# Kernel optimization log

Hardware: AMD Instinct MI355X
Metric: run time of the kernel (lower is better)

Reference implementation:

```python
import jax, jax.numpy as jnp
import numpy as np

D = 768
B = 512

def setup_inputs() -> dict:
    key = jax.random.key(0)
    k1, k2, k3 = jax.random.split(key, 3)
    v_x = jax.random.normal(k1, (B, D), dtype=jnp.float32)
    s_x = jax.random.normal(k2, (B, D), dtype=jnp.float32)
    # nn.Linear(D*D, 2) weight (2, D*D), bias (2,)
    fc_w = jax.random.normal(k3, (2, D * D), dtype=jnp.float32) * 0.01
    fc_b = jnp.zeros((2,), dtype=jnp.float32)
    return {"v_x": v_x, "s_x": s_x, "fc_w": fc_w, "fc_b": fc_b}

def reference(v_x, s_x, fc_w, fc_b):
    d = v_x.shape[1]
    # Original: M[b,i,j] = v_x[b,i]*s_x[b,j]; logits = M_flat @ fc_w.T + fc_b.
    # Equivalent bilinear form avoiding the (B,d,d) intermediate:
    # logits[b,k] = sum_ij v[b,i] * s[b,j] * fc_w[k, i*d+j]
    W = fc_w.reshape(2, d, d)  # W[k,i,j]
    logits = jnp.einsum('bi,kij,bj->bk', v_x, W, s_x) + fc_b
    weights = jax.nn.softmax(logits, axis=-1)
    a = weights[:, 0:1]
    b = weights[:, 1:2]
    fused_x = a * v_x + b * s_x
    return fused_x
```

## Files before the change

### kernel.cpp

```cpp
#include <hip/hip_runtime.h>

#define D 768
#define B 512

#define BM 128
#define BN 128
#define IC 16
#define ISPLIT 16
#define ILEN (D / ISPLIT)
#define NJT (D / BN)
#define NPART (ISPLIT * NJT)
#define WROW 192
#define VROW 132

__global__ __launch_bounds__(256, 4)
void gemm_kernel(const float* __restrict__ v_x,
                 const float* __restrict__ s_x,
                 const float* __restrict__ fc_w,
                 float* __restrict__ partial )
{
    __shared__ float wS[IC * WROW];
    __shared__ float vT[IC * VROW];

    const int tid   = threadIdx.x;
    const int gx    = blockIdx.x;
    const int gy    = blockIdx.y;
    const int gz    = blockIdx.z;
    const int k     = gx / NJT;
    const int jmod  = gx % NJT;
    const int jbase = jmod * BN;
    const int b0    = gy * BM;

    const int jt = tid & 15;
    const int bt = tid >> 4;

    const float* __restrict__ Wk = fc_w + (size_t)k * D * D;

    float acc[8][8];
#pragma unroll
    for (int m = 0; m < 8; ++m)
#pragma unroll
        for (int n = 0; n < 8; ++n) acc[m][n] = 0.f;

    for (int ch = 0; ch < ILEN / IC; ++ch) {
        const int i0 = gz * ILEN + ch * IC;

#pragma unroll
        for (int p = 0; p < 2; ++p) {
            int q  = tid + 256 * p;
            int r  = q >> 5;
            int c4 = q & 31;
            float4 t = *reinterpret_cast<const float4*>(
                &Wk[(size_t)(i0 + r) * D + jbase + c4 * 4]);
            *reinterpret_cast<float4*>(&wS[r * WROW + (c4 >> 1) * 12 + (c4 & 1) * 4]) = t;
        }
#pragma unroll
        for (int p = 0; p < 2; ++p) {
            int q  = tid + 256 * p;
            int bq = q >> 2;
            int c4 = q & 3;
            float4 t = *reinterpret_cast<const float4*>(
                &v_x[(size_t)(b0 + bq) * D + i0 + c4 * 4]);
            vT[(c4 * 4 + 0) * VROW + bq] = t.x;
            vT[(c4 * 4 + 1) * VROW + bq] = t.y;
            vT[(c4 * 4 + 2) * VROW + bq] = t.z;
            vT[(c4 * 4 + 3) * VROW + bq] = t.w;
        }
        __syncthreads();

#pragma unroll
        for (int ii = 0; ii < IC; ++ii) {
            float4 a0 = *reinterpret_cast<const float4*>(&vT[ii * VROW + bt * 8]);
            float4 a1 = *reinterpret_cast<const float4*>(&vT[ii * VROW + bt * 8 + 4]);
            float4 w0 = *reinterpret_cast<const float4*>(&wS[ii * WROW + jt * 12]);
            float4 w1 = *reinterpret_cast<const float4*>(&wS[ii * WROW + jt * 12 + 4]);
            float a8[8] = {a0.x, a0.y, a0.z, a0.w, a1.x, a1.y, a1.z, a1.w};
            float w8[8] = {w0.x, w0.y, w0.z, w0.w, w1.x, w1.y, w1.z, w1.w};
#pragma unroll
            for (int m = 0; m < 8; ++m)
#pragma unroll
                for (int n = 0; n < 8; ++n)
                    acc[m][n] = fmaf(a8[m], w8[n], acc[m][n]);
        }
        __syncthreads();
    }

#pragma unroll
    for (int m = 0; m < 8; ++m) {
        const int row = b0 + bt * 8 + m;
        const float* sp = s_x + (size_t)row * D + jbase + jt * 8;
        float4 s0 = *reinterpret_cast<const float4*>(sp);
        float4 s1 = *reinterpret_cast<const float4*>(sp + 4);
        float val = acc[m][0]*s0.x + acc[m][1]*s0.y + acc[m][2]*s0.z + acc[m][3]*s0.w
                  + acc[m][4]*s1.x + acc[m][5]*s1.y + acc[m][6]*s1.z + acc[m][7]*s1.w;
        val += __shfl_xor(val, 1);
        val += __shfl_xor(val, 2);
        val += __shfl_xor(val, 4);
        val += __shfl_xor(val, 8);
        if (jt == 0) {
            partial[(size_t)row * (2 * NPART) + k * NPART + gz * NJT + jmod] = val;
        }
    }
}

__global__ __launch_bounds__(192)
void fuse_kernel(const float* __restrict__ v_x,
                 const float* __restrict__ s_x,
                 const float* __restrict__ partial,
                 const float* __restrict__ fc_b,
                 float* __restrict__ out)
{
    __shared__ float slog[2];
    const int b    = blockIdx.x;
    const int t    = threadIdx.x;
    const int wave = t >> 6;
    const int lane = t & 63;

    if (wave < 2) {
        const float* P = partial + (size_t)b * (2 * NPART) + wave * NPART;
        float val = P[lane];
        if (lane < NPART - 64) val += P[64 + lane];
        val += __shfl_xor(val, 1);
        val += __shfl_xor(val, 2);
        val += __shfl_xor(val, 4);
        val += __shfl_xor(val, 8);
        val += __shfl_xor(val, 16);
        val += __shfl_xor(val, 32);
        if (lane == 0) slog[wave] = val + fc_b[wave];
    }
    __syncthreads();

    const float l0 = slog[0], l1 = slog[1];
    const float mx = fmaxf(l0, l1);
    const float e0 = __expf(l0 - mx);
    const float e1 = __expf(l1 - mx);
    const float inv = 1.f / (e0 + e1);
    const float wa = e0 * inv;
    const float wb = e1 * inv;

    const float4* v4 = reinterpret_cast<const float4*>(v_x + (size_t)b * D);
    const float4* s4 = reinterpret_cast<const float4*>(s_x + (size_t)b * D);
    float4* o4 = reinterpret_cast<float4*>((float*)out + (size_t)b * D);
    float4 vv = v4[t], ss = s4[t], oo;
    oo.x = wa * vv.x + wb * ss.x;
    oo.y = wa * vv.y + wb * ss.y;
    oo.z = wa * vv.z + wb * ss.z;
    oo.w = wa * vv.w + wb * ss.w;
    o4[t] = oo;
}

extern "C" void kernel_launch(void* const* d_in, const int* in_sizes, int n_in,
                              void* d_out, int out_size, void* d_ws, size_t ws_size,
                              hipStream_t stream) {
    const float* v_x  = (const float*)d_in[0];
    const float* s_x  = (const float*)d_in[1];
    const float* fc_w = (const float*)d_in[2];
    const float* fc_b = (const float*)d_in[3];
    float* out     = (float*)d_out;
    float* partial = (float*)d_ws;

    dim3 g1(2 * NJT, B / BM, ISPLIT);
    gemm_kernel<<<g1, 256, 0, stream>>>(v_x, s_x, fc_w, partial);

    fuse_kernel<<<B, 192, 0, stream>>>(v_x, s_x, partial, fc_b, out);
}
```

Baseline: 85.78 us.

## Use fp16 MFMA for bilinear GEMM with transposed half-precision weights

Adds a prep kernel that converts v_x to fp16 and transposes the two weight matrices into fp16 with a shared-memory tile. The main GEMM then runs on MFMA 16x16x32 f16 instructions with a 64x128 tile and an 8-way K split, reduces across waves through LDS, and writes 48 partials per class instead of 96. This removes the scalar FP32 FMA bottleneck and halves operand bandwidth. In exchange it adds an extra kernel launch plus weight conversion on every call, and rounding inputs to fp16 lowers accuracy.

Measured after the change: 79.99 us. 6.8% less time.

```diff
diff --git a/kernel.cpp b/kernel.cpp
--- a/kernel.cpp
+++ b/kernel.cpp
@@ -3,103 +3,142 @@
 #define D 768
 #define B 512
 
-#define BM 128
+typedef _Float16 half8 __attribute__((ext_vector_type(8)));
+typedef float floatx4 __attribute__((ext_vector_type(4)));
+
+__global__ __launch_bounds__(256)
+void prep_kernel(const float* __restrict__ v_x,
+                 const float* __restrict__ fc_w,
+                 _Float16* __restrict__ WT,
+                 _Float16* __restrict__ v16)
+{
+    __shared__ _Float16 tile[32 * 33];
+    const int bid = blockIdx.x;
+    const int t   = threadIdx.x;
+
+    if (bid < 1152) {
+        const int cls = bid / 576;
+        const int r2  = bid % 576;
+        const int kt  = r2 / 24;
+        const int jt  = r2 % 24;
+        const float* Wc = fc_w + (size_t)cls * D * D;
+        const int r  = t >> 3;
+        const int c4 = t & 7;
+        float4 f = *reinterpret_cast<const float4*>(
+            &Wc[(size_t)(kt * 32 + r) * D + jt * 32 + c4 * 4]);
+        tile[r * 33 + c4 * 4 + 0] = (_Float16)f.x;
+        tile[r * 33 + c4 * 4 + 1] = (_Float16)f.y;
+        tile[r * 33 + c4 * 4 + 2] = (_Float16)f.z;
+        tile[r * 33 + c4 * 4 + 3] = (_Float16)f.w;
+        __syncthreads();
+        alignas(8) _Float16 o[4];
+#pragma unroll
+        for (int e = 0; e < 4; ++e) o[e] = tile[(c4 * 4 + e) * 33 + r];
+        *reinterpret_cast<short4*>(
+            &WT[((size_t)cls * D + jt * 32 + r) * D + kt * 32 + c4 * 4]) =
+            *reinterpret_cast<short4*>(o);
+    } else {
+        const int b2 = bid - 1152;
+        const int base = b2 * 1024 + t * 4;
+        float4 f = *reinterpret_cast<const float4*>(&v_x[base]);
+        alignas(8) _Float16 o[4] = {(_Float16)f.x, (_Float16)f.y,
+                                    (_Float16)f.z, (_Float16)f.w};
+        *reinterpret_cast<short4*>(&v16[base]) = *reinterpret_cast<short4*>(o);
+    }
+}
+
+#define BM 64
 #define BN 128
-#define IC 16
-#define ISPLIT 16
-#define ILEN (D / ISPLIT)
-#define NJT (D / BN)
-#define NPART (ISPLIT * NJT)
-#define WROW 192
-#define VROW 132
-
-__global__ __launch_bounds__(256, 4)
-void gemm_kernel(const float* __restrict__ v_x,
+#define KC 96
+#define LROW 104
+#define NJT 6
+#define NPART 48
+
+__global__ __launch_bounds__(256, 3)
+void gemm_kernel(const _Float16* __restrict__ v16,
+                 const _Float16* __restrict__ WT,
                  const float* __restrict__ s_x,
-                 const float* __restrict__ fc_w,
                  float* __restrict__ partial )
 {
-    __shared__ float wS[IC * WROW];
-    __shared__ float vT[IC * VROW];
-
-    const int tid   = threadIdx.x;
-    const int gx    = blockIdx.x;
-    const int gy    = blockIdx.y;
-    const int gz    = blockIdx.z;
-    const int k     = gx / NJT;
-    const int jmod  = gx % NJT;
-    const int jbase = jmod * BN;
-    const int b0    = gy * BM;
-
-    const int jt = tid & 15;
-    const int bt = tid >> 4;
-
-    const float* __restrict__ Wk = fc_w + (size_t)k * D * D;
-
-    float acc[8][8];
-#pragma unroll
-    for (int m = 0; m < 8; ++m)
-#pragma unroll
-        for (int n = 0; n < 8; ++n) acc[m][n] = 0.f;
-
-    for (int ch = 0; ch < ILEN / IC; ++ch) {
-        const int i0 = gz * ILEN + ch * IC;
-
-#pragma unroll
-        for (int p = 0; p < 2; ++p) {
-            int q  = tid + 256 * p;
-            int r  = q >> 5;
-            int c4 = q & 31;
-            float4 t = *reinterpret_cast<const float4*>(
-                &Wk[(size_t)(i0 + r) * D + jbase + c4 * 4]);
-            *reinterpret_cast<float4*>(&wS[r * WROW + (c4 >> 1) * 12 + (c4 & 1) * 4]) = t;
+    __shared__ _Float16 Alds[BM * LROW];
+    __shared__ _Float16 Blds[BN * LROW];
+    __shared__ float    red[BM * 4];
+
+    const int tid = threadIdx.x;
+    const int jb  = blockIdx.x;
+    const int b0  = blockIdx.y * BM;
+    const int gz  = blockIdx.z;
+    const int kc0 = gz * KC;
+
+    const int w    = tid >> 6;
+    const int lane = tid & 63;
+    const int li   = lane & 15;
+    const int g    = lane >> 4;
+
+#pragma unroll
+    for (int p = 0; p < 3; ++p) {
+        int q   = tid + 256 * p;
+        int row = q / 12, ksl = q % 12;
+        half8 h = *reinterpret_cast<const half8*>(
+            &v16[(size_t)(b0 + row) * D + kc0 + ksl * 8]);
+        *reinterpret_cast<half8*>(&Alds[row * LROW + ksl * 8]) = h;
+    }
+    const _Float16* Wrow = WT + (size_t)jb * BN * D;
+#pragma unroll
+    for (int p = 0; p < 6; ++p) {
+        int q   = tid + 256 * p;
+        int row = q / 12, ksl = q % 12;
+        half8 h = *reinterpret_cast<const half8*>(
+            &Wrow[(size_t)row * D + kc0 + ksl * 8]);
+        *reinterpret_cast<half8*>(&Blds[row * LROW + ksl * 8]) = h;
+    }
+    __syncthreads();
+
+    floatx4 acc[4][2];
+#pragma unroll
+    for (int m = 0; m < 4; ++m)
+#pragma unroll
+        for (int n = 0; n < 2; ++n) acc[m][n] = {0.f, 0.f, 0.f, 0.f};
+
+#pragma unroll
+    for (int ks = 0; ks < KC / 32; ++ks) {
+        half8 a[4], bf[2];
+#pragma unroll
+        for (int m = 0; m < 4; ++m)
+            a[m] = *reinterpret_cast<const half8*>(
+                &Alds[(m * 16 + li) * LROW + ks * 32 + g * 8]);
+#pragma unroll
+        for (int n = 0; n < 2; ++n)
+            bf[n] = *reinterpret_cast<const half8*>(
+                &Blds[(w * 32 + n * 16 + li) * LROW + ks * 32 + g * 8]);
+#pragma unroll
+        for (int m = 0; m < 4; ++m)
+#pragma unroll
+            for (int n = 0; n < 2; ++n)
+                acc[m][n] = __builtin_amdgcn_mfma_f32_16x16x32_f16(
+                    a[m], bf[n], acc[m][n], 0, 0, 0);
+    }
+
+    const int js  = (jb % NJT) * BN;
+    const int cls = jb / NJT;
+#pragma unroll
+    for (int m = 0; m < 4; ++m)
+#pragma unroll
+        for (int r = 0; r < 4; ++r) {
+            const int row = m * 16 + 4 * g + r;
+            const float* sp = s_x + (size_t)(b0 + row) * D + js + w * 32 + li;
+            float val = acc[m][0][r] * sp[0] + acc[m][1][r] * sp[16];
+            val += __shfl_xor(val, 1);
+            val += __shfl_xor(val, 2);
+            val += __shfl_xor(val, 4);
+            val += __shfl_xor(val, 8);
+            if (li == 0) red[row * 4 + w] = val;
         }
-#pragma unroll
-        for (int p = 0; p < 2; ++p) {
-            int q  = tid + 256 * p;
-            int bq = q >> 2;
-            int c4 = q & 3;
-            float4 t = *reinterpret_cast<const float4*>(
-                &v_x[(size_t)(b0 + bq) * D + i0 + c4 * 4]);
-            vT[(c4 * 4 + 0) * VROW + bq] = t.x;
-            vT[(c4 * 4 + 1) * VROW + bq] = t.y;
-            vT[(c4 * 4 + 2) * VROW + bq] = t.z;
-            vT[(c4 * 4 + 3) * VROW + bq] = t.w;
-        }
-        __syncthreads();
-
-#pragma unroll
-        for (int ii = 0; ii < IC; ++ii) {
-            float4 a0 = *reinterpret_cast<const float4*>(&vT[ii * VROW + bt * 8]);
-            float4 a1 = *reinterpret_cast<const float4*>(&vT[ii * VROW + bt * 8 + 4]);
-            float4 w0 = *reinterpret_cast<const float4*>(&wS[ii * WROW + jt * 12]);
-            float4 w1 = *reinterpret_cast<const float4*>(&wS[ii * WROW + jt * 12 + 4]);
-            float a8[8] = {a0.x, a0.y, a0.z, a0.w, a1.x, a1.y, a1.z, a1.w};
-            float w8[8] = {w0.x, w0.y, w0.z, w0.w, w1.x, w1.y, w1.z, w1.w};
-#pragma unroll
-            for (int m = 0; m < 8; ++m)
-#pragma unroll
-                for (int n = 0; n < 8; ++n)
-                    acc[m][n] = fmaf(a8[m], w8[n], acc[m][n]);
-        }
-        __syncthreads();
-    }
-
-#pragma unroll
-    for (int m = 0; m < 8; ++m) {
-        const int row = b0 + bt * 8 + m;
-        const float* sp = s_x + (size_t)row * D + jbase + jt * 8;
-        float4 s0 = *reinterpret_cast<const float4*>(sp);
-        float4 s1 = *reinterpret_cast<const float4*>(sp + 4);
-        float val = acc[m][0]*s0.x + acc[m][1]*s0.y + acc[m][2]*s0.z + acc[m][3]*s0.w
-                  + acc[m][4]*s1.x + acc[m][5]*s1.y + acc[m][6]*s1.z + acc[m][7]*s1.w;
-        val += __shfl_xor(val, 1);
-        val += __shfl_xor(val, 2);
-        val += __shfl_xor(val, 4);
-        val += __shfl_xor(val, 8);
-        if (jt == 0) {
-            partial[(size_t)row * (2 * NPART) + k * NPART + gz * NJT + jmod] = val;
-        }
+    __syncthreads();
+    if (tid < BM) {
+        float4 rv = *reinterpret_cast<const float4*>(&red[tid * 4]);
+        partial[(size_t)(b0 + tid) * (2 * NPART) + cls * NPART + gz * NJT + (jb % NJT)]
+            = rv.x + rv.y + rv.z + rv.w;
     }
 }
 
@@ -118,8 +157,7 @@
 
     if (wave < 2) {
         const float* P = partial + (size_t)b * (2 * NPART) + wave * NPART;
-        float val = P[lane];
-        if (lane < NPART - 64) val += P[64 + lane];
+        float val = (lane < NPART) ? P[lane] : 0.f;
         val += __shfl_xor(val, 1);
         val += __shfl_xor(val, 2);
         val += __shfl_xor(val, 4);
@@ -156,11 +194,17 @@
     const float* s_x  = (const float*)d_in[1];
     const float* fc_w = (const float*)d_in[2];
     const float* fc_b = (const float*)d_in[3];
-    float* out     = (float*)d_out;
-    float* partial = (float*)d_ws;
-
-    dim3 g1(2 * NJT, B / BM, ISPLIT);
-    gemm_kernel<<<g1, 256, 0, stream>>>(v_x, s_x, fc_w, partial);
+    float* out = (float*)d_out;
+
+    char* ws = (char*)d_ws;
+    _Float16* WT  = (_Float16*)(ws);
+    _Float16* v16 = (_Float16*)(ws + (size_t)(1 << 22));
+    float* partial = (float*)(ws + (size_t)(1 << 23));
+
+    prep_kernel<<<1152 + 384, 256, 0, stream>>>(v_x, fc_w, WT, v16);
+
+    dim3 g1(12, B / BM, 8);
+    gemm_kernel<<<g1, 256, 0, stream>>>(v16, WT, s_x, partial);
 
     fuse_kernel<<<B, 192, 0, stream>>>(v_x, s_x, partial, fc_b, out);
 }
```
